# Kernel optimization log

Measured on AMD Instinct MI355X. Metric: run time of the kernel, lower is better.

The kernel has to match this reference:

```python
import jax, jax.numpy as jnp
import numpy as np

H = 512      # hidden_size (hardcoded in __init__)
WD = 1024    # word_dim (hardcoded)
V = 4096     # len(i2w)+4
B, S, T = 256, 80, 28


def setup_inputs() -> dict:
    key = jax.random.key(0)
    ks = jax.random.split(key, 14)

    def gl(k, shape, fan_in):
        return (jax.random.normal(k, shape, jnp.float32) / np.sqrt(fan_in)).astype(jnp.float32)

    return {
        "encoder_last_hidden_state": jax.random.normal(ks[0], (1, B, H), jnp.float32),
        "encoder_output": jax.random.normal(ks[1], (B, S, H), jnp.float32),
        "targets": jax.random.randint(ks[2], (B, T), 0, V, dtype=jnp.int32),
        # embedding table
        "embedding": gl(ks[3], (V, WD), WD),
        # attention MLP (4 stacked linears, no activations, per the source)
        "W1": gl(ks[4], (2 * H, H), 2 * H), "b1": jnp.zeros((H,), jnp.float32),
        "W2": gl(ks[5], (H, H), H), "b2": jnp.zeros((H,), jnp.float32),
        "W3": gl(ks[6], (H, H), H), "b3": jnp.zeros((H,), jnp.float32),
        "W4": gl(ks[7], (H, H), H), "b4": jnp.zeros((H,), jnp.float32),
        "Ww": gl(ks[8], (H, 1), H),
        # GRU (input = hidden_size + word_dim = 1536), PyTorch gate order r,z,n
        "W_ih": gl(ks[9], (3 * H, H + WD), H + WD), "b_ih": jnp.zeros((3 * H,), jnp.float32),
        "W_hh": gl(ks[10], (3 * H, H), H), "b_hh": jnp.zeros((3 * H,), jnp.float32),
        # output projection
        "Wo": gl(ks[11], (H, V), H), "bo": jnp.zeros((V,), jnp.float32),
    }


def reference(encoder_last_hidden_state, encoder_output, targets, embedding,
              W1, b1, W2, b2, W3, b3, W4, b4, Ww,
              W_ih, b_ih, W_hh, b_hh, Wo, bo):
    n_steps = targets.shape[1] - 1  # seq_len - 1 decode steps

    def attention(h, enc):
        # h: (B,H) decoder hidden; enc: (B,S,H)
        hs = jnp.broadcast_to(h[:, None, :], enc.shape)
        m = jnp.concatenate([enc, hs], axis=-1)          # (B,S,2H)
        x = m @ W1 + b1
        x = x @ W2 + b2
        x = x @ W3 + b3
        x = x @ W4 + b4
        attw = jax.nn.softmax((x @ Ww)[..., 0], axis=1)  # (B,S)
        return jnp.einsum('bs,bsh->bh', attw, enc)       # context (B,H)

    def gru_cell(x, h):
        gi = x @ W_ih.T + b_ih
        gh = h @ W_hh.T + b_hh
        ir, iz, inn = jnp.split(gi, 3, axis=-1)
        hr, hz, hn = jnp.split(gh, 3, axis=-1)
        r = jax.nn.sigmoid(ir + hr)
        z = jax.nn.sigmoid(iz + hz)
        n = jnp.tanh(inn + r * hn)
        return (1.0 - z) * n + z * h

    h0 = encoder_last_hidden_state[0]                    # (B,H)
    w0 = jnp.ones((encoder_output.shape[0],), jnp.int32) # <BOS> = 1

    def step(carry, _):
        h, w = carry
        emb = embedding[w]                               # (B,WD)
        ctx = attention(h, encoder_output)               # (B,H)
        x = jnp.concatenate([emb, ctx], axis=-1)         # (B,WD+H)
        hn = gru_cell(x, h)
        logits = hn @ Wo + bo                            # (B,V)
        wn = jnp.argmax(logits, axis=-1).astype(jnp.int32)
        return (hn, wn), logits

    _, logits_seq = jax.lax.scan(step, (h0, w0), None, length=n_steps)
    seq_logProb = jnp.swapaxes(logits_seq, 0, 1)         # (B, T-1, V)
    seq_predictions = jnp.argmax(seq_logProb, axis=-1)
    return seq_logProb, seq_predictions
```

## Files before the change

kernel.cpp:

```cpp
#include <hip/hip_runtime.h>

#define B_ 256
#define S_ 80
#define H_ 512
#define V_ 4096
#define NSTEP 27

typedef unsigned short u16;
typedef __attribute__((ext_vector_type(8))) short short8v;
typedef __attribute__((ext_vector_type(4))) float f32x4;
typedef __attribute__((ext_vector_type(4))) unsigned short ushort4v;

#define MFMA_(a,b,c) __builtin_amdgcn_mfma_f32_16x16x32_bf16(a,b,c,0,0,0)
#define MFMA3(acc, ah, al, bh, bl) do{ acc = MFMA_(ah,bh,acc); acc = MFMA_(ah,bl,acc); acc = MFMA_(al,bh,acc);}while(0)

__device__ __forceinline__ unsigned fkey(float v){
    unsigned u = __float_as_uint(v);
    return (u & 0x80000000u) ? ~u : (u | 0x80000000u);
}
__device__ __forceinline__ u16 bf16_rne(float f){
    unsigned u = __float_as_uint(f);
    return (u16)((u + 0x7FFFu + ((u >> 16) & 1u)) >> 16);
}
__device__ __forceinline__ void split_f4(float4 v, ushort4v& hi, ushort4v& lo){
    float arr[4] = {v.x, v.y, v.z, v.w};
    ushort4v h, l;
#pragma unroll
    for (int i = 0; i < 4; ++i){
        u16 hb = bf16_rne(arr[i]);
        h[i] = hb;
        l[i] = bf16_rne(arr[i] - __uint_as_float(((unsigned)hb) << 16));
    }
    hi = h; lo = l;
}

__global__ __launch_bounds__(64) void matvec512(const float* __restrict__ W,
                                                const float* __restrict__ v,
                                                float* __restrict__ out){
    int row = blockIdx.x, lane = threadIdx.x;
    const float* wr = W + row * 512;
    float s = 0.f;
#pragma unroll
    for (int i = 0; i < 8; ++i) s += wr[lane + 64*i] * v[lane + 64*i];
#pragma unroll
    for (int off = 32; off; off >>= 1) s += __shfl_xor(s, off);
    if (lane == 0) out[row] = s;
}

__global__ __launch_bounds__(256) void score_kernel(const float* __restrict__ enc,
                                                    const float* __restrict__ weff,
                                                    float* __restrict__ scores){
    int wv = threadIdx.x >> 6, lane = threadIdx.x & 63;
    int p = blockIdx.x * 4 + wv;
    const float* e = enc + (size_t)p * 512;
    float s = 0.f;
#pragma unroll
    for (int i = 0; i < 8; ++i) s += e[lane + 64*i] * weff[lane + 64*i];
#pragma unroll
    for (int off = 32; off; off >>= 1) s += __shfl_xor(s, off);
    if (lane == 0) scores[p] = s;
}

__global__ __launch_bounds__(512) void softmax_ctx(const float* __restrict__ enc,
                                                   const float* __restrict__ scores,
                                                   float* __restrict__ ctx){
    __shared__ float att[S_];
    int b = blockIdx.x, tid = threadIdx.x;
    if (tid < S_) att[tid] = scores[b*S_ + tid];
    __syncthreads();
    if (tid == 0){
        float mx = att[0];
        for (int s = 1; s < S_; ++s) mx = fmaxf(mx, att[s]);
        float sum = 0.f;
        for (int s = 0; s < S_; ++s){ float e = expf(att[s] - mx); att[s] = e; sum += e; }
        float inv = 1.f / sum;
        for (int s = 0; s < S_; ++s) att[s] *= inv;
    }
    __syncthreads();
    float a = 0.f;
    const float* eb = enc + (size_t)b * (S_*H_);
    for (int s = 0; s < S_; ++s) a += att[s] * eb[s*H_ + tid];
    ctx[b*H_ + tid] = a;
}

template<int TM>
__global__ __launch_bounds__(256) void gemm_abt(const float* __restrict__ A, int lda,
                                                const float* __restrict__ Bm, int ldb,
                                                const float* __restrict__ bias,
                                                float* __restrict__ C, int ldc, int K){
    constexpr int RPT = TM / 16;
    __shared__ float As[16][TM + 4];
    __shared__ float Bs[16][64 + 4];
    int m0 = blockIdx.x * TM, n0 = blockIdx.y * 64;
    int tid = threadIdx.x;
    int lk = tid & 15, lr = tid >> 4;
    int tx = tid & 15, ty = tid >> 4;
    float c[RPT][4] = {};
    for (int k0 = 0; k0 < K; k0 += 16){
#pragma unroll
        for (int i = 0; i < RPT; ++i)
            As[lk][lr*RPT + i] = A[(size_t)(m0 + lr*RPT + i)*lda + k0 + lk];
#pragma unroll
        for (int i = 0; i < 4; ++i)
            Bs[lk][lr*4 + i] = Bm[(size_t)(n0 + lr*4 + i)*ldb + k0 + lk];
        __syncthreads();
#pragma unroll
        for (int k = 0; k < 16; ++k){
            float b4[4];
            *(float4*)b4 = *(const float4*)&Bs[k][tx*4];
#pragma unroll
            for (int i = 0; i < RPT; ++i){
                float a = As[k][ty*RPT + i];
#pragma unroll
                for (int j = 0; j < 4; ++j) c[i][j] += a * b4[j];
            }
        }
        __syncthreads();
    }
#pragma unroll
    for (int j = 0; j < 4; ++j){
        float bb = bias ? bias[n0 + tx*4 + j] : 0.f;
#pragma unroll
        for (int i = 0; i < RPT; ++i)
            C[(size_t)(m0 + ty*RPT + i)*ldc + n0 + tx*4 + j] = c[i][j] + bb;
    }
}

__global__ __launch_bounds__(256) void prep_all(
    const float* __restrict__ Whh, const float* __restrict__ Wo,
    const float* __restrict__ emb, const float* __restrict__ Wih,
    const float* __restrict__ elhs,
    u16* __restrict__ WhhHi, u16* __restrict__ WhhLo,
    u16* __restrict__ WoThi, u16* __restrict__ WoTlo,
    u16* __restrict__ EmbHi, u16* __restrict__ EmbLo,
    u16* __restrict__ WihLHi, u16* __restrict__ WihLLo,
    u16* __restrict__ Sh, u16* __restrict__ Sl,
    unsigned* __restrict__ zp, int nz)
{
    __shared__ float T[64][65];
    int b = blockIdx.x, tid = threadIdx.x;
    if (b < 768){
        int idx = (b*256 + tid)*4;
        float4 v = *(const float4*)&Whh[idx];
        ushort4v h,l; split_f4(v,h,l);
        *(ushort4v*)&WhhHi[idx]=h; *(ushort4v*)&WhhLo[idx]=l;
    } else if (b < 1280){
        int lb = b - 768;
        int k0 = (lb & 7)*64, n0 = (lb >> 3)*64;
#pragma unroll
        for (int i = 0; i < 16; ++i){
            int idx = tid + i*256;
            int kk = idx >> 6, nn = idx & 63;
            T[kk][nn] = Wo[(size_t)(k0+kk)*4096 + n0+nn];
        }
        __syncthreads();
#pragma unroll
        for (int i = 0; i < 16; ++i){
            int idx = tid + i*256;
            int nn = idx >> 6, kk = idx & 63;
            float v = T[kk][nn];
            u16 hi = bf16_rne(v);
            u16 lo = bf16_rne(v - __uint_as_float(((unsigned)hi) << 16));
            size_t o = (size_t)(n0+nn)*512 + k0+kk;
            WoThi[o] = hi; WoTlo[o] = lo;
        }
    } else if (b < 5376){
        int idx = ((b-1280)*256 + tid)*4;
        float4 v = *(const float4*)&emb[idx];
        ushort4v h,l; split_f4(v,h,l);
        *(ushort4v*)&EmbHi[idx]=h; *(ushort4v*)&EmbLo[idx]=l;
    } else if (b < 6912){
        int id = ((b-5376)*256 + tid)*4;
        int r = id >> 10, c = id & 1023;
        float4 v = *(const float4*)&Wih[(size_t)r*1536 + c];
        ushort4v h,l; split_f4(v,h,l);
        *(ushort4v*)&WihLHi[id]=h; *(ushort4v*)&WihLLo[id]=l;
    } else if (b < 7040){
        int idx = ((b-6912)*256 + tid)*4;
        float4 v = *(const float4*)&elhs[idx];
        ushort4v h,l; split_f4(v,h,l);
        *(ushort4v*)&Sh[idx]=h; *(ushort4v*)&Sl[idx]=l;
    } else {
        int i = ((b-7040)*256 + tid)*4;
        if (i < nz){ zp[i]=0u; zp[i+1]=0u; zp[i+2]=0u; zp[i+3]=0u; }
    }
}

__global__ __launch_bounds__(256) void eproj_u16(const u16* __restrict__ Ahi, const u16* __restrict__ Alo,
                                                 const u16* __restrict__ Bhi, const u16* __restrict__ Blo,
                                                 float* __restrict__ C){
    __shared__ u16 Ah[2048], Al[2048], Bh[4096], Bl[4096];
    int n0 = blockIdx.x * 128, m0 = blockIdx.y * 64;
    int tid = threadIdx.x, lane = tid & 63, wid = tid >> 6;
    int wy = wid & 1, wx = wid >> 1;
    int l15 = lane & 15, rg = lane >> 4, lk = rg * 8;
    int ar = tid >> 2, ak8 = (tid & 3) * 8;

    const u16* gAh = Ahi + (size_t)(m0 + ar)*1024 + ak8;
    const u16* gAl = Alo + (size_t)(m0 + ar)*1024 + ak8;
    const u16* gBh0 = Bhi + (size_t)(n0 + ar)*1024 + ak8;
    const u16* gBl0 = Blo + (size_t)(n0 + ar)*1024 + ak8;
    const u16* gBh1 = gBh0 + (size_t)64*1024;
    const u16* gBl1 = gBl0 + (size_t)64*1024;

    short8v rAh = *(const short8v*)gAh;
    short8v rAl = *(const short8v*)gAl;
    short8v rBh0 = *(const short8v*)gBh0;
    short8v rBl0 = *(const short8v*)gBl0;
    short8v rBh1 = *(const short8v*)gBh1;
    short8v rBl1 = *(const short8v*)gBl1;

    f32x4 acc[2][4] = {};
    for (int k0 = 0; k0 < 1024; k0 += 32){
        __syncthreads();
        *(short8v*)&Ah[tid*8] = rAh;
        *(short8v*)&Al[tid*8] = rAl;
        *(short8v*)&Bh[tid*8] = rBh0;
        *(short8v*)&Bl[tid*8] = rBl0;
        *(short8v*)&Bh[2048 + tid*8] = rBh1;
        *(short8v*)&Bl[2048 + tid*8] = rBl1;
        __syncthreads();
        if (k0 + 32 < 1024){
            rAh  = *(const short8v*)(gAh + k0 + 32);
            rAl  = *(const short8v*)(gAl + k0 + 32);
            rBh0 = *(const short8v*)(gBh0 + k0 + 32);
            rBl0 = *(const short8v*)(gBl0 + k0 + 32);
            rBh1 = *(const short8v*)(gBh1 + k0 + 32);
            rBl1 = *(const short8v*)(gBl1 + k0 + 32);
        }
        short8v afh[2], afl[2];
        afh[0] = *(const short8v*)&Ah[(wy*32 +  0 + l15)*32 + lk];
        afh[1] = *(const short8v*)&Ah[(wy*32 + 16 + l15)*32 + lk];
        afl[0] = *(const short8v*)&Al[(wy*32 +  0 + l15)*32 + lk];
        afl[1] = *(const short8v*)&Al[(wy*32 + 16 + l15)*32 + lk];
#pragma unroll
        for (int nf = 0; nf < 4; ++nf){
            short8v bfh = *(const short8v*)&Bh[(wx*64 + nf*16 + l15)*32 + lk];
            short8v bfl = *(const short8v*)&Bl[(wx*64 + nf*16 + l15)*32 + lk];
            MFMA3(acc[0][nf], afh[0], afl[0], bfh, bfl);
            MFMA3(acc[1][nf], afh[1], afl[1], bfh, bfl);
        }
    }
    int col0 = n0 + wx*64 + l15;
#pragma unroll
    for (int mf = 0; mf < 2; ++mf)
#pragma unroll
        for (int r = 0; r < 4; ++r){
            int row = m0 + wy*32 + mf*16 + rg*4 + r;
#pragma unroll
            for (int nf = 0; nf < 4; ++nf)
                C[(size_t)row*1536 + col0 + nf*16] = acc[mf][nf][r];
        }
}


__global__ __launch_bounds__(256) void gru_pointwise(
    const float* __restrict__ gh, const float* __restrict__ Eproj,
    const float* __restrict__ gictx, const float* __restrict__ bhh,
    const float* __restrict__ hprev, float* __restrict__ hnext,
    u16* __restrict__ Sh, u16* __restrict__ Sl,
    const unsigned long long* __restrict__ Pprev,
    float* __restrict__ preds, int t)
{
    int tid = threadIdx.x;
    int row = blockIdx.x * 2 + (tid >> 7);
    int jj = (tid & 127) * 4;
    int w = 1;
    if (t > 0){
        w = 4095 - (int)(Pprev[row] & 0xFFFFFFFFull);
        if (w < 0) w = 0; if (w > 4095) w = 4095;
        if (jj == 0) preds[row*NSTEP + (t-1)] = (float)w;
    }
    const float* gr = gh + (size_t)row * 1536;
    const float* ep = Eproj + (size_t)w * 1536;
    const float* gc = gictx + (size_t)row * 1536;
    float4 g0 = *(const float4*)&gr[jj];
    float4 g1 = *(const float4*)&gr[512 + jj];
    float4 g2 = *(const float4*)&gr[1024 + jj];
    float4 e0 = *(const float4*)&ep[jj];
    float4 e1 = *(const float4*)&ep[512 + jj];
    float4 e2 = *(const float4*)&ep[1024 + jj];
    float4 c0 = *(const float4*)&gc[jj];
    float4 c1 = *(const float4*)&gc[512 + jj];
    float4 c2 = *(const float4*)&gc[1024 + jj];
    float4 b0 = *(const float4*)&bhh[jj];
    float4 b1 = *(const float4*)&bhh[512 + jj];
    float4 b2 = *(const float4*)&bhh[1024 + jj];
    float4 ho = *(const float4*)&hprev[(size_t)row*512 + jj];
    const float* G0 = (const float*)&g0; const float* G1 = (const float*)&g1;
    const float* G2 = (const float*)&g2;
    const float* E0 = (const float*)&e0; const float* E1 = (const float*)&e1;
    const float* E2 = (const float*)&e2;
    const float* C0 = (const float*)&c0; const float* C1 = (const float*)&c1;
    const float* C2 = (const float*)&c2;
    const float* B0 = (const float*)&b0; const float* B1 = (const float*)&b1;
    const float* B2 = (const float*)&b2;
    const float* HO = (const float*)&ho;
    float4 res;
    float* R = (float*)&res;
#pragma unroll
    for (int i = 0; i < 4; ++i){
        float gir = E0[i] + C0[i] + G0[i] + B0[i];
        float giz = E1[i] + C1[i] + G1[i] + B1[i];
        float gin = E2[i] + C2[i];
        float rr = 1.f / (1.f + expf(-gir));
        float zz = 1.f / (1.f + expf(-giz));
        float nn = tanhf(gin + rr * (G2[i] + B2[i]));
        R[i] = (1.f - zz)*nn + zz*HO[i];
    }
    size_t o = (size_t)row*512 + jj;
    *(float4*)&hnext[o] = res;
    ushort4v h4, l4; split_f4(res, h4, l4);
    *(ushort4v*)&Sh[o] = h4;
    *(ushort4v*)&Sl[o] = l4;
}

__global__ __launch_bounds__(256) void step_mm(
    const u16* __restrict__ Ahg, const u16* __restrict__ Alg,
    const u16* __restrict__ WoHi, const u16* __restrict__ WoLo,
    const u16* __restrict__ WhhHi, const u16* __restrict__ WhhLo,
    const float* __restrict__ bo,
    float* __restrict__ logits, unsigned long long* __restrict__ Pcur,
    float* __restrict__ gh_out, int n_logits)
{
    __shared__ u16 Ah[2048], Al[2048], Bh[4096], Bl[4096];
    int m0 = blockIdx.x * 64;
    int nt = blockIdx.y;
    bool isL = nt < n_logits;
    int nbase = (isL ? nt : nt - n_logits) * 128;
    const u16* Bhg = isL ? WoHi : WhhHi;
    const u16* Blg = isL ? WoLo : WhhLo;
    int tid = threadIdx.x, lane = tid & 63, wid = tid >> 6;
    int wy = wid & 1, wx = wid >> 1;
    int l15 = lane & 15, rg = lane >> 4, lk = rg * 8;
    int ar = tid >> 2, ak8 = (tid & 3) * 8;

    const u16* gAh = Ahg + (size_t)(m0 + ar)*512 + ak8;
    const u16* gAl = Alg + (size_t)(m0 + ar)*512 + ak8;
    const u16* gBh0 = Bhg + (size_t)(nbase + ar)*512 + ak8;
    const u16* gBl0 = Blg + (size_t)(nbase + ar)*512 + ak8;
    const u16* gBh1 = gBh0 + (size_t)64*512;
    const u16* gBl1 = gBl0 + (size_t)64*512;

    short8v rAh = *(const short8v*)gAh;
    short8v rAl = *(const short8v*)gAl;
    short8v rBh0 = *(const short8v*)gBh0;
    short8v rBl0 = *(const short8v*)gBl0;
    short8v rBh1 = *(const short8v*)gBh1;
    short8v rBl1 = *(const short8v*)gBl1;

    f32x4 acc[2][4] = {};
    for (int k0 = 0; k0 < 512; k0 += 32){
        __syncthreads();
        *(short8v*)&Ah[tid*8] = rAh;
        *(short8v*)&Al[tid*8] = rAl;
        *(short8v*)&Bh[tid*8] = rBh0;
        *(short8v*)&Bl[tid*8] = rBl0;
        *(short8v*)&Bh[2048 + tid*8] = rBh1;
        *(short8v*)&Bl[2048 + tid*8] = rBl1;
        __syncthreads();
        if (k0 + 32 < 512){
            rAh  = *(const short8v*)(gAh + k0 + 32);
            rAl  = *(const short8v*)(gAl + k0 + 32);
            rBh0 = *(const short8v*)(gBh0 + k0 + 32);
            rBl0 = *(const short8v*)(gBl0 + k0 + 32);
            rBh1 = *(const short8v*)(gBh1 + k0 + 32);
            rBl1 = *(const short8v*)(gBl1 + k0 + 32);
        }
        short8v afh[2], afl[2];
        afh[0] = *(const short8v*)&Ah[(wy*32 +  0 + l15)*32 + lk];
        afh[1] = *(const short8v*)&Ah[(wy*32 + 16 + l15)*32 + lk];
        afl[0] = *(const short8v*)&Al[(wy*32 +  0 + l15)*32 + lk];
        afl[1] = *(const short8v*)&Al[(wy*32 + 16 + l15)*32 + lk];
#pragma unroll
        for (int nf = 0; nf < 4; ++nf){
            short8v bfh = *(const short8v*)&Bh[(wx*64 + nf*16 + l15)*32 + lk];
            short8v bfl = *(const short8v*)&Bl[(wx*64 + nf*16 + l15)*32 + lk];
            MFMA3(acc[0][nf], afh[0], afl[0], bfh, bfl);
            MFMA3(acc[1][nf], afh[1], afl[1], bfh, bfl);
        }
    }
    if (isL){
        float bov[4];
#pragma unroll
        for (int nf = 0; nf < 4; ++nf) bov[nf] = bo[nbase + wx*64 + nf*16 + l15];
#pragma unroll
        for (int mf = 0; mf < 2; ++mf){
#pragma unroll
            for (int r = 0; r < 4; ++r){
                int row = m0 + wy*32 + mf*16 + rg*4 + r;
                float* crow = logits + (size_t)row * (NSTEP * (size_t)V_);
                unsigned long long best = 0ULL;
#pragma unroll
                for (int nf = 0; nf < 4; ++nf){
                    int col = nbase + wx*64 + nf*16 + l15;
                    float v = acc[mf][nf][r] + bov[nf];
                    crow[col] = v;
                    unsigned long long key = ((unsigned long long)fkey(v) << 32) | (unsigned)(4095 - col);
                    if (key > best) best = key;
                }
#pragma unroll
                for (int off = 1; off < 16; off <<= 1){
                    unsigned long long o = __shfl_xor(best, off);
                    if (o > best) best = o;
                }
                if (l15 == 0) atomicMax(&Pcur[row], best);
            }
        }
    } else {
        int col0 = nbase + wx*64 + l15;
#pragma unroll
        for (int mf = 0; mf < 2; ++mf)
#pragma unroll
            for (int r = 0; r < 4; ++r){
                int row = m0 + wy*32 + mf*16 + rg*4 + r;
#pragma unroll
                for (int nf = 0; nf < 4; ++nf)
                    gh_out[(size_t)row*1536 + col0 + nf*16] = acc[mf][nf][r];
            }
    }
}

__global__ __launch_bounds__(256) void final_pred(const unsigned long long* __restrict__ P,
                                                  float* __restrict__ preds){
    int b = threadIdx.x;
    int w = 4095 - (int)(P[b] & 0xFFFFFFFFull);
    if (w < 0) w = 0; if (w > 4095) w = 4095;
    preds[b*NSTEP + (NSTEP-1)] = (float)w;
}

extern "C" void kernel_launch(void* const* d_in, const int* in_sizes, int n_in,
                              void* d_out, int out_size, void* d_ws, size_t ws_size,
                              hipStream_t stream){
    const float* elhs = (const float*)d_in[0];
    const float* enc  = (const float*)d_in[1];
    const float* emb  = (const float*)d_in[3];
    const float* W1   = (const float*)d_in[4];
    const float* W2   = (const float*)d_in[6];
    const float* W3   = (const float*)d_in[8];
    const float* W4   = (const float*)d_in[10];
    const float* Ww   = (const float*)d_in[12];
    const float* Wih  = (const float*)d_in[13];
    const float* bih  = (const float*)d_in[14];
    const float* Whh  = (const float*)d_in[15];
    const float* bhh  = (const float*)d_in[16];
    const float* Wo   = (const float*)d_in[17];
    const float* bo   = (const float*)d_in[18];

    float* out = (float*)d_out;
    float* preds = out + (size_t)B_ * NSTEP * V_;

    float* ws = (float*)d_ws;
    float* Eproj  = ws;  ws += (size_t)V_ * 1536;
    float* gictx  = ws;  ws += (size_t)B_ * 1536;
    float* ctx    = ws;  ws += B_ * H_;
    float* scores = ws;  ws += B_ * S_;
    float* t1     = ws;  ws += 512;
    float* t2     = ws;  ws += 512;
    float* weff   = ws;  ws += 512;
    float* Hf     = ws;  ws += 2 * B_ * H_;
    float* ghbuf  = ws;  ws += B_ * 1536;
    u16* WoT_hi = (u16*)ws;  ws += (size_t)V_ * 512 / 2;
    u16* WoT_lo = (u16*)ws;  ws += (size_t)V_ * 512 / 2;
    u16* WhhHi  = (u16*)ws;  ws += 1536 * 512 / 2;
    u16* WhhLo  = (u16*)ws;  ws += 1536 * 512 / 2;
    u16* Sh     = (u16*)ws;  ws += B_ * H_ / 2;
    u16* Sl     = (u16*)ws;  ws += B_ * H_ / 2;
    unsigned long long* P = (unsigned long long*)ws;

    u16* EmbHi  = (u16*)d_out;
    u16* EmbLo  = EmbHi + (size_t)V_*1024;
    u16* WihLHi = EmbLo + (size_t)V_*1024;
    u16* WihLLo = WihLHi + (size_t)1536*1024;

    prep_all<<<7054, 256, 0, stream>>>(Whh, Wo, emb, Wih, elhs,
                                       WhhHi, WhhLo, WoT_hi, WoT_lo,
                                       EmbHi, EmbLo, WihLHi, WihLLo,
                                       Sh, Sl, (unsigned*)P, NSTEP*256*2);

    matvec512<<<512, 64, 0, stream>>>(W4, Ww, t1);
    matvec512<<<512, 64, 0, stream>>>(W3, t1, t2);
    matvec512<<<512, 64, 0, stream>>>(W2, t2, t1);
    matvec512<<<512, 64, 0, stream>>>(W1, t1, weff);
    score_kernel<<<(B_*S_)/4, 256, 0, stream>>>(enc, weff, scores);
    softmax_ctx<<<B_, 512, 0, stream>>>(enc, scores, ctx);
    { dim3 g(B_/32, 1536/64);
      gemm_abt<32><<<g, 256, 0, stream>>>(ctx, 512, Wih + 1024, 1536, bih, gictx, 1536, 512); }
    { dim3 g(1536/128, V_/64);
      eproj_u16<<<g, 256, 0, stream>>>(EmbHi, EmbLo, WihLHi, WihLLo, Eproj); }

    { dim3 g(4, 12);
      step_mm<<<g, 256, 0, stream>>>(Sh, Sl, WoT_hi, WoT_lo, WhhHi, WhhLo, bo,
                                     out, P, ghbuf, 0); }

    for (int t = 0; t < NSTEP; ++t){
        const float* hr = (t == 0) ? elhs : (Hf + (size_t)((t-1) & 1) * (B_*H_));
        float*       hw = Hf + (size_t)(t & 1) * (B_*H_);
        const unsigned long long* Pprev = P + (size_t)(t > 0 ? t-1 : 0) * 256;
        gru_pointwise<<<128, 256, 0, stream>>>(ghbuf, Eproj, gictx, bhh, hr, hw,
                                               Sh, Sl, Pprev, preds, t);
        dim3 g(4, 32 + 12);
        step_mm<<<g, 256, 0, stream>>>(Sh, Sl, WoT_hi, WoT_lo, WhhHi, WhhLo, bo,
                                       out + (size_t)t * V_, P + (size_t)t*256, ghbuf, 32);
    }
    final_pred<<<1, 256, 0, stream>>>(P + (size_t)(NSTEP-1)*256, preds);
}
```

Measured before the change: 763.2 us.

## Shrink step_mm N-tile, double-buffer LDS, and fuse attention score with softmax

```diff
diff --git a/kernel.cpp b/kernel.cpp
--- a/kernel.cpp
+++ b/kernel.cpp
@@ -47,26 +47,25 @@
     if (lane == 0) out[row] = s;
 }
 
-__global__ __launch_bounds__(256) void score_kernel(const float* __restrict__ enc,
-                                                    const float* __restrict__ weff,
-                                                    float* __restrict__ scores){
-    int wv = threadIdx.x >> 6, lane = threadIdx.x & 63;
-    int p = blockIdx.x * 4 + wv;
-    const float* e = enc + (size_t)p * 512;
-    float s = 0.f;
-#pragma unroll
-    for (int i = 0; i < 8; ++i) s += e[lane + 64*i] * weff[lane + 64*i];
-#pragma unroll
-    for (int off = 32; off; off >>= 1) s += __shfl_xor(s, off);
-    if (lane == 0) scores[p] = s;
-}
-
-__global__ __launch_bounds__(512) void softmax_ctx(const float* __restrict__ enc,
-                                                   const float* __restrict__ scores,
-                                                   float* __restrict__ ctx){
+__global__ __launch_bounds__(512) void attn_ctx(const float* __restrict__ enc,
+                                                const float* __restrict__ weff,
+                                                float* __restrict__ ctx){
     __shared__ float att[S_];
     int b = blockIdx.x, tid = threadIdx.x;
-    if (tid < S_) att[tid] = scores[b*S_ + tid];
+    int wv = tid >> 6, lane = tid & 63;
+    float w8[8];
+#pragma unroll
+    for (int i = 0; i < 8; ++i) w8[i] = weff[lane + 64*i];
+    const float* eb = enc + (size_t)b * (S_*H_);
+    for (int s = wv; s < S_; s += 8){
+        const float* e = eb + s*512;
+        float acc = 0.f;
+#pragma unroll
+        for (int i = 0; i < 8; ++i) acc += e[lane + 64*i] * w8[i];
+#pragma unroll
+        for (int off = 32; off; off >>= 1) acc += __shfl_xor(acc, off);
+        if (lane == 0) att[s] = acc;
+    }
     __syncthreads();
     if (tid == 0){
         float mx = att[0];
@@ -78,9 +77,8 @@
     }
     __syncthreads();
     float a = 0.f;
-    const float* eb = enc + (size_t)b * (S_*H_);
-    for (int s = 0; s < S_; ++s) a += att[s] * eb[s*H_ + tid];
-    ctx[b*H_ + tid] = a;
+    for (int s = 0; s < S_; ++s) a += att[s] * eb[s*512 + tid];
+    ctx[b*512 + tid] = a;
 }
 
 template<int TM>
@@ -254,7 +252,7 @@
 }
 
 
-__global__ __launch_bounds__(256) void gru_pointwise(
+__global__ __launch_bounds__(128) void gru_pointwise(
     const float* __restrict__ gh, const float* __restrict__ Eproj,
     const float* __restrict__ gictx, const float* __restrict__ bhh,
     const float* __restrict__ hprev, float* __restrict__ hnext,
@@ -263,13 +261,13 @@
     float* __restrict__ preds, int t)
 {
     int tid = threadIdx.x;
-    int row = blockIdx.x * 2 + (tid >> 7);
-    int jj = (tid & 127) * 4;
+    int row = blockIdx.x;
+    int jj = tid * 4;
     int w = 1;
     if (t > 0){
         w = 4095 - (int)(Pprev[row] & 0xFFFFFFFFull);
         if (w < 0) w = 0; if (w > 4095) w = 4095;
-        if (jj == 0) preds[row*NSTEP + (t-1)] = (float)w;
+        if (tid == 0) preds[row*NSTEP + (t-1)] = (float)w;
     }
     const float* gr = gh + (size_t)row * 1536;
     const float* ep = Eproj + (size_t)w * 1536;
@@ -323,82 +321,81 @@
     float* __restrict__ logits, unsigned long long* __restrict__ Pcur,
     float* __restrict__ gh_out, int n_logits)
 {
-    __shared__ u16 Ah[2048], Al[2048], Bh[4096], Bl[4096];
+    __shared__ u16 Ah[2][2048], Al[2][2048], Bh[2][2048], Bl[2][2048];
     int m0 = blockIdx.x * 64;
     int nt = blockIdx.y;
     bool isL = nt < n_logits;
-    int nbase = (isL ? nt : nt - n_logits) * 128;
+    int nbase = (isL ? nt : nt - n_logits) * 64;
     const u16* Bhg = isL ? WoHi : WhhHi;
     const u16* Blg = isL ? WoLo : WhhLo;
     int tid = threadIdx.x, lane = tid & 63, wid = tid >> 6;
     int wy = wid & 1, wx = wid >> 1;
     int l15 = lane & 15, rg = lane >> 4, lk = rg * 8;
-    int ar = tid >> 2, ak8 = (tid & 3) * 8;
-
-    const u16* gAh = Ahg + (size_t)(m0 + ar)*512 + ak8;
-    const u16* gAl = Alg + (size_t)(m0 + ar)*512 + ak8;
-    const u16* gBh0 = Bhg + (size_t)(nbase + ar)*512 + ak8;
-    const u16* gBl0 = Blg + (size_t)(nbase + ar)*512 + ak8;
-    const u16* gBh1 = gBh0 + (size_t)64*512;
-    const u16* gBl1 = gBl0 + (size_t)64*512;
-
-    short8v rAh = *(const short8v*)gAh;
-    short8v rAl = *(const short8v*)gAl;
-    short8v rBh0 = *(const short8v*)gBh0;
-    short8v rBl0 = *(const short8v*)gBl0;
-    short8v rBh1 = *(const short8v*)gBh1;
-    short8v rBl1 = *(const short8v*)gBl1;
-
-    f32x4 acc[2][4] = {};
+    int sr = tid >> 2, sk8 = (tid & 3) * 8;
+
+    const u16* gAh = Ahg + (size_t)(m0 + sr)*512 + sk8;
+    const u16* gAl = Alg + (size_t)(m0 + sr)*512 + sk8;
+    const u16* gBh = Bhg + (size_t)(nbase + sr)*512 + sk8;
+    const u16* gBl = Blg + (size_t)(nbase + sr)*512 + sk8;
+
+    *(short8v*)&Ah[0][tid*8] = *(const short8v*)gAh;
+    *(short8v*)&Al[0][tid*8] = *(const short8v*)gAl;
+    *(short8v*)&Bh[0][tid*8] = *(const short8v*)gBh;
+    *(short8v*)&Bl[0][tid*8] = *(const short8v*)gBl;
+    short8v r1a = *(const short8v*)(gAh + 32), r1b = *(const short8v*)(gAl + 32);
+    short8v r1c = *(const short8v*)(gBh + 32), r1d = *(const short8v*)(gBl + 32);
+    short8v r2a = *(const short8v*)(gAh + 64), r2b = *(const short8v*)(gAl + 64);
+    short8v r2c = *(const short8v*)(gBh + 64), r2d = *(const short8v*)(gBl + 64);
+    __syncthreads();
+
+    f32x4 acc[2][2] = {};
+    int p = 0;
     for (int k0 = 0; k0 < 512; k0 += 32){
+        if (k0 + 32 < 512){
+            *(short8v*)&Ah[p^1][tid*8] = r1a;
+            *(short8v*)&Al[p^1][tid*8] = r1b;
+            *(short8v*)&Bh[p^1][tid*8] = r1c;
+            *(short8v*)&Bl[p^1][tid*8] = r1d;
+            r1a = r2a; r1b = r2b; r1c = r2c; r1d = r2d;
+            if (k0 + 96 < 512){
+                r2a = *(const short8v*)(gAh + k0 + 96);
+                r2b = *(const short8v*)(gAl + k0 + 96);
+                r2c = *(const short8v*)(gBh + k0 + 96);
+                r2d = *(const short8v*)(gBl + k0 + 96);
+            }
+        }
+        short8v afh0 = *(const short8v*)&Ah[p][(wy*32 +  0 + l15)*32 + lk];
+        short8v afh1 = *(const short8v*)&Ah[p][(wy*32 + 16 + l15)*32 + lk];
+        short8v afl0 = *(const short8v*)&Al[p][(wy*32 +  0 + l15)*32 + lk];
+        short8v afl1 = *(const short8v*)&Al[p][(wy*32 + 16 + l15)*32 + lk];
+        short8v bfh0 = *(const short8v*)&Bh[p][(wx*32 +  0 + l15)*32 + lk];
+        short8v bfh1 = *(const short8v*)&Bh[p][(wx*32 + 16 + l15)*32 + lk];
+        short8v bfl0 = *(const short8v*)&Bl[p][(wx*32 +  0 + l15)*32 + lk];
+        short8v bfl1 = *(const short8v*)&Bl[p][(wx*32 + 16 + l15)*32 + lk];
+        MFMA3(acc[0][0], afh0, afl0, bfh0, bfl0);
+        MFMA3(acc[0][1], afh0, afl0, bfh1, bfl1);
+        MFMA3(acc[1][0], afh1, afl1, bfh0, bfl0);
+        MFMA3(acc[1][1], afh1, afl1, bfh1, bfl1);
         __syncthreads();
-        *(short8v*)&Ah[tid*8] = rAh;
-        *(short8v*)&Al[tid*8] = rAl;
-        *(short8v*)&Bh[tid*8] = rBh0;
-        *(short8v*)&Bl[tid*8] = rBl0;
-        *(short8v*)&Bh[2048 + tid*8] = rBh1;
-        *(short8v*)&Bl[2048 + tid*8] = rBl1;
-        __syncthreads();
-        if (k0 + 32 < 512){
-            rAh  = *(const short8v*)(gAh + k0 + 32);
-            rAl  = *(const short8v*)(gAl + k0 + 32);
-            rBh0 = *(const short8v*)(gBh0 + k0 + 32);
-            rBl0 = *(const short8v*)(gBl0 + k0 + 32);
-            rBh1 = *(const short8v*)(gBh1 + k0 + 32);
-            rBl1 = *(const short8v*)(gBl1 + k0 + 32);
-        }
-        short8v afh[2], afl[2];
-        afh[0] = *(const short8v*)&Ah[(wy*32 +  0 + l15)*32 + lk];
-        afh[1] = *(const short8v*)&Ah[(wy*32 + 16 + l15)*32 + lk];
-        afl[0] = *(const short8v*)&Al[(wy*32 +  0 + l15)*32 + lk];
-        afl[1] = *(const short8v*)&Al[(wy*32 + 16 + l15)*32 + lk];
-#pragma unroll
-        for (int nf = 0; nf < 4; ++nf){
-            short8v bfh = *(const short8v*)&Bh[(wx*64 + nf*16 + l15)*32 + lk];
-            short8v bfl = *(const short8v*)&Bl[(wx*64 + nf*16 + l15)*32 + lk];
-            MFMA3(acc[0][nf], afh[0], afl[0], bfh, bfl);
-            MFMA3(acc[1][nf], afh[1], afl[1], bfh, bfl);
-        }
-    }
+        p ^= 1;
+    }
+
+    int col0 = nbase + wx*32 + l15;
     if (isL){
-        float bov[4];
-#pragma unroll
-        for (int nf = 0; nf < 4; ++nf) bov[nf] = bo[nbase + wx*64 + nf*16 + l15];
+        float bo0 = bo[col0], bo1 = bo[col0 + 16];
 #pragma unroll
         for (int mf = 0; mf < 2; ++mf){
 #pragma unroll
             for (int r = 0; r < 4; ++r){
                 int row = m0 + wy*32 + mf*16 + rg*4 + r;
+                float v0 = acc[mf][0][r] + bo0;
+                float v1 = acc[mf][1][r] + bo1;
                 float* crow = logits + (size_t)row * (NSTEP * (size_t)V_);
-                unsigned long long best = 0ULL;
-#pragma unroll
-                for (int nf = 0; nf < 4; ++nf){
-                    int col = nbase + wx*64 + nf*16 + l15;
-                    float v = acc[mf][nf][r] + bov[nf];
-                    crow[col] = v;
-                    unsigned long long key = ((unsigned long long)fkey(v) << 32) | (unsigned)(4095 - col);
-                    if (key > best) best = key;
-                }
+                crow[col0]      = v0;
+                crow[col0 + 16] = v1;
+                unsigned long long k0_ = ((unsigned long long)fkey(v0) << 32) | (unsigned)(4095 - col0);
+                unsigned long long k1_ = ((unsigned long long)fkey(v1) << 32) | (unsigned)(4095 - (col0+16));
+                unsigned long long best = k0_ > k1_ ? k0_ : k1_;
 #pragma unroll
                 for (int off = 1; off < 16; off <<= 1){
                     unsigned long long o = __shfl_xor(best, off);
@@ -408,15 +405,13 @@
             }
         }
     } else {
-        int col0 = nbase + wx*64 + l15;
 #pragma unroll
         for (int mf = 0; mf < 2; ++mf)
 #pragma unroll
             for (int r = 0; r < 4; ++r){
                 int row = m0 + wy*32 + mf*16 + rg*4 + r;
-#pragma unroll
-                for (int nf = 0; nf < 4; ++nf)
-                    gh_out[(size_t)row*1536 + col0 + nf*16] = acc[mf][nf][r];
+                gh_out[(size_t)row*1536 + col0]      = acc[mf][0][r];
+                gh_out[(size_t)row*1536 + col0 + 16] = acc[mf][1][r];
             }
     }
 }
@@ -454,7 +449,6 @@
     float* Eproj  = ws;  ws += (size_t)V_ * 1536;
     float* gictx  = ws;  ws += (size_t)B_ * 1536;
     float* ctx    = ws;  ws += B_ * H_;
-    float* scores = ws;  ws += B_ * S_;
     float* t1     = ws;  ws += 512;
     float* t2     = ws;  ws += 512;
     float* weff   = ws;  ws += 512;
@@ -482,14 +476,13 @@
     matvec512<<<512, 64, 0, stream>>>(W3, t1, t2);
     matvec512<<<512, 64, 0, stream>>>(W2, t2, t1);
     matvec512<<<512, 64, 0, stream>>>(W1, t1, weff);
-    score_kernel<<<(B_*S_)/4, 256, 0, stream>>>(enc, weff, scores);
-    softmax_ctx<<<B_, 512, 0, stream>>>(enc, scores, ctx);
+    attn_ctx<<<B_, 512, 0, stream>>>(enc, weff, ctx);
     { dim3 g(B_/32, 1536/64);
       gemm_abt<32><<<g, 256, 0, stream>>>(ctx, 512, Wih + 1024, 1536, bih, gictx, 1536, 512); }
     { dim3 g(1536/128, V_/64);
       eproj_u16<<<g, 256, 0, stream>>>(EmbHi, EmbLo, WihLHi, WihLLo, Eproj); }
 
-    { dim3 g(4, 12);
+    { dim3 g(4, 24);
       step_mm<<<g, 256, 0, stream>>>(Sh, Sl, WoT_hi, WoT_lo, WhhHi, WhhLo, bo,
                                      out, P, ghbuf, 0); }
 
@@ -497,11 +490,11 @@
         const float* hr = (t == 0) ? elhs : (Hf + (size_t)((t-1) & 1) * (B_*H_));
         float*       hw = Hf + (size_t)(t & 1) * (B_*H_);
         const unsigned long long* Pprev = P + (size_t)(t > 0 ? t-1 : 0) * 256;
-        gru_pointwise<<<128, 256, 0, stream>>>(ghbuf, Eproj, gictx, bhh, hr, hw,
+        gru_pointwise<<<256, 128, 0, stream>>>(ghbuf, Eproj, gictx, bhh, hr, hw,
                                                Sh, Sl, Pprev, preds, t);
-        dim3 g(4, 32 + 12);
+        dim3 g(4, 64 + 24);
         step_mm<<<g, 256, 0, stream>>>(Sh, Sl, WoT_hi, WoT_lo, WhhHi, WhhLo, bo,
-                                       out + (size_t)t * V_, P + (size_t)t*256, ghbuf, 32);
+                                       out + (size_t)t * V_, P + (size_t)t*256, ghbuf, 64);
     }
     final_pred<<<1, 256, 0, stream>>>(P + (size_t)(NSTEP-1)*256, preds);
 }
```

New measurement: 746.5 us. 2.2% less time.
